# Kernel optimization log

Hardware: AMD Instinct MI355X
Metric: run time of the kernel (lower is better)

The kernel has to match this reference:

```python
import jax, jax.numpy as jnp
import numpy as np

N = 100000
E = 1600000
IN_F = 128
H_F = 128


def _sage_layer(h, weights, src, dst, W_self, b_self, W_neigh):
    # message: w_e * h[src]  -> [E, F]
    m = h[src] * weights[:, None]
    # segment-mean over destination nodes (DGL fn.mean divides by in-degree)
    s = jax.ops.segment_sum(m, dst, num_segments=N)
    deg = jax.ops.segment_sum(jnp.ones((E,), h.dtype), dst, num_segments=N)
    neigh = s / jnp.maximum(deg, 1.0)[:, None]
    # DGL SAGEConv('mean'): fc_self(h) + fc_neigh(neigh); bias lives in fc_self
    return h @ W_self.T + b_self + neigh @ W_neigh.T


def setup_inputs() -> dict:
    key = jax.random.key(0)
    ks = jax.random.split(key, 10)
    scale_in = 1.0 / np.sqrt(IN_F)
    scale_h = 1.0 / np.sqrt(H_F)
    return {
        "in_feat": jax.random.normal(ks[0], (N, IN_F), jnp.float32),
        "weights": jax.random.uniform(ks[1], (E,), jnp.float32),
        "src": jax.random.randint(ks[2], (E,), 0, N),
        "dst": jax.random.randint(ks[3], (E,), 0, N),
        "W_self1": jax.random.normal(ks[4], (H_F, IN_F), jnp.float32) * scale_in,
        "b_self1": jnp.zeros((H_F,), jnp.float32),
        "W_neigh1": jax.random.normal(ks[5], (H_F, IN_F), jnp.float32) * scale_in,
        "W_self2": jax.random.normal(ks[6], (H_F, H_F), jnp.float32) * scale_h,
        "b_self2": jnp.zeros((H_F,), jnp.float32),
        "W_neigh2": jax.random.normal(ks[7], (H_F, H_F), jnp.float32) * scale_h,
    }


def reference(in_feat, weights, src, dst, W_self1, b_self1, W_neigh1, W_self2, b_self2, W_neigh2):
    h = _sage_layer(in_feat, weights, src, dst, W_self1, b_self1, W_neigh1)
    h = jax.nn.relu(h)
    h = _sage_layer(h, weights, src, dst, W_self2, b_self2, W_neigh2)
    return h
```

## Files before the change

### kernel.cpp

```cpp
#include <hip/hip_runtime.h>


#define NN 100000
#define NE 1600000
#define F 128

#define SCAN_BS 1024
#define NBLK ((NN + SCAN_BS - 1) / SCAN_BS)

#define NPB 512
#define NBUK ((NN + NPB - 1) / NPB)
#define EPB 4096
#define NBLK3 ((NE + EPB - 1) / EPB)

static const size_t CNT_OFF   = 0;
static const size_t ROW_OFF   = 400000;
static const size_t BSUM_OFF  = 800016;
static const size_t EDGE_OFF  = 804112;
static const size_t WCAT1_OFF = 13604112;
static const size_t WCAT2_OFF = 13669648;
static const size_t SBF_OFF   = 13735184;
static const size_t H1BF_OFF  = 39335184;
static const size_t WS_NEED   = 64935184;

static const size_t FB_S_OFF = 524288;

typedef __attribute__((ext_vector_type(8))) short short8;
typedef __attribute__((ext_vector_type(4))) float float4v;

__device__ __forceinline__ float bf2f(unsigned int u16) {
    unsigned int x = u16 << 16;
    float f;
    __builtin_memcpy(&f, &x, 4);
    return f;
}
__device__ __forceinline__ unsigned int f2bf(float f) {
    unsigned int x;
    __builtin_memcpy(&x, &f, 4);
    unsigned int r = x + 0x7FFFu + ((x >> 16) & 1u);
    return r >> 16;
}


__global__ __launch_bounds__(256) void count_kernel(const int* __restrict__ dst,
                                                    int* __restrict__ cnt) {
    int e = blockIdx.x * 256 + threadIdx.x;
    if (e < NE) atomicAdd(&cnt[dst[e]], 1);
}

__global__ __launch_bounds__(256) void scan1_kernel(const int* __restrict__ cnt,
                                                    int* __restrict__ part,
                                                    int* __restrict__ bsum) {
    __shared__ int ts[256];
    int t = threadIdx.x;
    int base = blockIdx.x * SCAN_BS + t * 4;
    int c0 = (base     < NN) ? cnt[base]     : 0;
    int c1 = (base + 1 < NN) ? cnt[base + 1] : 0;
    int c2 = (base + 2 < NN) ? cnt[base + 2] : 0;
    int c3 = (base + 3 < NN) ? cnt[base + 3] : 0;
    int sum = c0 + c1 + c2 + c3;
    ts[t] = sum;
    __syncthreads();
    for (int off = 1; off < 256; off <<= 1) {
        int u = (t >= off) ? ts[t - off] : 0;
        __syncthreads();
        ts[t] += u;
        __syncthreads();
    }
    int excl = ts[t] - sum;
    if (t == 255) bsum[blockIdx.x] = ts[255];
    if (base     < NN) part[base]     = excl;
    if (base + 1 < NN) part[base + 1] = excl + c0;
    if (base + 2 < NN) part[base + 2] = excl + c0 + c1;
    if (base + 3 < NN) part[base + 3] = excl + c0 + c1 + c2;
}

__global__ __launch_bounds__(128) void scan2_kernel(int* __restrict__ bsum) {
    __shared__ int ts[128];
    int t = threadIdx.x;
    int v = (t < NBLK) ? bsum[t] : 0;
    ts[t] = v;
    __syncthreads();
    for (int off = 1; off < 128; off <<= 1) {
        int u = (t >= off) ? ts[t - off] : 0;
        __syncthreads();
        ts[t] += u;
        __syncthreads();
    }
    if (t < NBLK) bsum[t] = ts[t] - v;
}

__global__ __launch_bounds__(256) void scan3_kernel(int* __restrict__ part,
                                                    const int* __restrict__ bsum) {
    int i = blockIdx.x * 256 + threadIdx.x;
    if (i < NN) part[i] += bsum[i / SCAN_BS];
    if (i == 0) part[NN] = NE;
}


__global__ void bcur_init(const int* __restrict__ row, int* __restrict__ bcur) {
    int b = threadIdx.x;
    if (b < NBUK) bcur[b] = row[b * NPB];
}

__global__ __launch_bounds__(256) void bscatter(const int* __restrict__ src,
                                                const int* __restrict__ dst,
                                                const float* __restrict__ w,
                                                int* __restrict__ bcur,
                                                int2* __restrict__ ebuf) {
    __shared__ int2 rec[EPB];
    __shared__ unsigned char bid[EPB];
    __shared__ int hist[NBUK];
    __shared__ int gbase[NBUK];
    __shared__ int cur[NBUK];

    int t = threadIdx.x;
    for (int i = t; i < NBUK; i += 256) { hist[i] = 0; cur[i] = 0; }
    __syncthreads();

    int base_e = blockIdx.x * EPB;
#pragma unroll
    for (int i = 0; i < 16; i++) {
        int idx = i * 256 + t;
        int e = base_e + idx;
        if (e < NE) {
            int d = dst[e];
            int b = d >> 9;
            int2 r;
            r.x = src[e] | ((d & 511) << 17);
            r.y = __float_as_int(w[e]);
            rec[idx] = r;
            bid[idx] = (unsigned char)b;
            atomicAdd(&hist[b], 1);
        } else {
            bid[idx] = 255;
        }
    }
    __syncthreads();

    for (int i = t; i < NBUK; i += 256)
        if (hist[i] > 0) gbase[i] = atomicAdd(&bcur[i], hist[i]);
    __syncthreads();

#pragma unroll
    for (int i = 0; i < 16; i++) {
        int idx = i * 256 + t;
        int b = bid[idx];
        if (b != 255) {
            int r = atomicAdd(&cur[b], 1);
            ebuf[gbase[b] + r] = rec[idx];
        }
    }
}

__global__ __launch_bounds__(256) void fine_fill(const int* __restrict__ row,
                                                 const int2* __restrict__ ebuf,
                                                 int2* __restrict__ edge) {
    __shared__ int lcur[NPB];
    int b = blockIdx.x;
    int t = threadIdx.x;
    int n0 = b * NPB;
    int n1 = min(n0 + NPB, NN);
    for (int i = t; i < n1 - n0; i += 256) lcur[i] = row[n0 + i];
    __syncthreads();
    int beg = row[n0], end = row[n1];
    for (int e = beg + t; e < end; e += 256) {
        int2 r = ebuf[e];
        int dl = (r.x >> 17) & 511;
        int pos = atomicAdd(&lcur[dl], 1);
        int2 o;
        o.x = r.x & 0x1FFFF;
        o.y = r.y;
        edge[pos] = o;
    }
}


__global__ __launch_bounds__(256) void wprep_kernel(const float* __restrict__ Ws,
                                                    const float* __restrict__ Wn,
                                                    unsigned short* __restrict__ wcat) {
    int idx = blockIdx.x * 256 + threadIdx.x;
    if (idx >= 128 * 256) return;
    int n = idx >> 8, k = idx & 255;
    float v = (k < 128) ? Ws[n * 128 + k] : Wn[n * 128 + (k - 128)];
    wcat[idx] = (unsigned short)f2bf(v);
}

__global__ __launch_bounds__(256) void conv_bf16(const float* __restrict__ in,
                                                 unsigned short* __restrict__ outbf) {
    size_t base = ((size_t)blockIdx.x * 256 + threadIdx.x) * 8;
    float4 a = *(const float4*)(in + base);
    float4 b = *(const float4*)(in + base + 4);
    uint4 p;
    p.x = f2bf(a.x) | (f2bf(a.y) << 16);
    p.y = f2bf(a.z) | (f2bf(a.w) << 16);
    p.z = f2bf(b.x) | (f2bf(b.y) << 16);
    p.w = f2bf(b.z) | (f2bf(b.w) << 16);
    *(uint4*)(outbf + base) = p;
}

__global__ __launch_bounds__(256) void gather_packed(const unsigned short* __restrict__ h,
                                                     const int* __restrict__ row,
                                                     const int2* __restrict__ edge,
                                                     unsigned short* __restrict__ sbf) {
    int t = threadIdx.x;
    int lane = t & 63;
    int n = blockIdx.x * 4 + (t >> 6);
    int beg = __builtin_amdgcn_readfirstlane(row[n]);
    int end = __builtin_amdgcn_readfirstlane(row[n + 1]);
    const unsigned int* hp = (const unsigned int*)h;

    float ax = 0.0f, ay = 0.0f;
    int e = beg;
    for (; e + 7 < end; e += 8) {
        int2 m[8];
#pragma unroll
        for (int i = 0; i < 8; i++) m[i] = edge[e + i];
        unsigned int p[8];
#pragma unroll
        for (int i = 0; i < 8; i++) p[i] = hp[(size_t)m[i].x * 64 + lane];
#pragma unroll
        for (int i = 0; i < 8; i++) {
            float wf = __int_as_float(m[i].y);
            ax += wf * bf2f(p[i] & 0xFFFFu);
            ay += wf * bf2f(p[i] >> 16);
        }
    }
    for (; e < end; e++) {
        int2 m0 = edge[e];
        unsigned int p0 = hp[(size_t)m0.x * 64 + lane];
        float wf = __int_as_float(m0.y);
        ax += wf * bf2f(p0 & 0xFFFFu);
        ay += wf * bf2f(p0 >> 16);
    }
    float invd = 1.0f / fmaxf((float)(end - beg), 1.0f);
    unsigned int outp = f2bf(ax * invd) | (f2bf(ay * invd) << 16);
    ((unsigned int*)sbf)[(size_t)n * 64 + lane] = outp;
}


__global__ __launch_bounds__(256) void mfma_gemm(
    const unsigned short* self_bf,
    const unsigned short* __restrict__ sbf,
    const unsigned short* __restrict__ wcat,
    const float* __restrict__ bias,
    unsigned short* out_bf,
    float* __restrict__ out_f32)
{
    __shared__ unsigned short Bs[128][256];

    int t = threadIdx.x;
    int l = t & 63;
    int w = t >> 6;
    int base = blockIdx.x * 128;
    int lane16 = l & 15;
    int quad = l >> 4;

    int r0 = base + w * 32 + lane16;
    int r1 = r0 + 16;
    int r0c = min(r0, NN - 1);
    int r1c = min(r1, NN - 1);

    const unsigned short* s0p = self_bf + (size_t)r0c * F + quad * 8;
    const unsigned short* s1p = self_bf + (size_t)r1c * F + quad * 8;
    const unsigned short* n0p = sbf     + (size_t)r0c * F + quad * 8;
    const unsigned short* n1p = sbf     + (size_t)r1c * F + quad * 8;

    short8 A0[8], A1[8];
#pragma unroll
    for (int kk = 0; kk < 4; kk++) {
        A0[kk]     = *(const short8*)(s0p + kk * 32);
        A1[kk]     = *(const short8*)(s1p + kk * 32);
        A0[4 + kk] = *(const short8*)(n0p + kk * 32);
        A1[4 + kk] = *(const short8*)(n1p + kk * 32);
    }

    uint4 sv[16];
#pragma unroll
    for (int i = 0; i < 16; i++) {
        int idx = i * 256 + t;
        sv[i] = *(const uint4*)(wcat + idx * 8);
    }
#pragma unroll
    for (int i = 0; i < 16; i++) {
        int idx = i * 256 + t;
        int r = idx >> 5;
        int c = (idx & 31) * 8;
        *(uint4*)&Bs[r][c] = sv[i];
    }
    __syncthreads();

    float4v acc0[8], acc1[8];
#pragma unroll
    for (int ct = 0; ct < 8; ct++) {
        acc0[ct] = (float4v){0.f, 0.f, 0.f, 0.f};
        acc1[ct] = (float4v){0.f, 0.f, 0.f, 0.f};
    }

#pragma unroll
    for (int half = 0; half < 2; half++) {
#pragma unroll
        for (int kk = 0; kk < 4; kk++) {
#pragma unroll
            for (int ct = 0; ct < 8; ct++) {
                short8 b = *(const short8*)&Bs[ct * 16 + lane16][half * 128 + kk * 32 + quad * 8];
                acc0[ct] = __builtin_amdgcn_mfma_f32_16x16x32_bf16(A0[half * 4 + kk], b, acc0[ct], 0, 0, 0);
                acc1[ct] = __builtin_amdgcn_mfma_f32_16x16x32_bf16(A1[half * 4 + kk], b, acc1[ct], 0, 0, 0);
            }
        }
    }

    int rowb0 = base + w * 32 + quad * 4;
    int rowb1 = rowb0 + 16;
#pragma unroll
    for (int ct = 0; ct < 8; ct++) {
        int col = ct * 16 + lane16;
        float bc = bias[col];
#pragma unroll
        for (int r = 0; r < 4; r++) {
            int g0 = rowb0 + r, g1 = rowb1 + r;
            float v0 = acc0[ct][r] + bc;
            float v1 = acc1[ct][r] + bc;
            if (out_bf) {
                v0 = fmaxf(v0, 0.0f);
                v1 = fmaxf(v1, 0.0f);
                if (g0 < NN) out_bf[(size_t)g0 * F + col] = (unsigned short)f2bf(v0);
                if (g1 < NN) out_bf[(size_t)g1 * F + col] = (unsigned short)f2bf(v1);
            } else {
                if (g0 < NN) out_f32[(size_t)g0 * F + col] = v0;
                if (g1 < NN) out_f32[(size_t)g1 * F + col] = v1;
            }
        }
    }
}


__global__ __launch_bounds__(256) void scatter_kernel(const float* __restrict__ h,
                                                      const float* __restrict__ w,
                                                      const int* __restrict__ src,
                                                      const int* __restrict__ dst,
                                                      float* __restrict__ s,
                                                      float* __restrict__ deg,
                                                      int add_deg) {
    int e = blockIdx.x * 4 + (threadIdx.x >> 6);
    int lane = threadIdx.x & 63;
    int sn = src[e];
    int dn = dst[e];
    float wf = w[e];
    float2 p = *(const float2*)(h + (size_t)sn * F + lane * 2);
    float* sp = s + (size_t)dn * F + lane * 2;
    unsafeAtomicAdd(sp,     wf * p.x);
    unsafeAtomicAdd(sp + 1, wf * p.y);
    if (add_deg && lane == 0) unsafeAtomicAdd(&deg[dn], 1.0f);
}

__global__ __launch_bounds__(256) void sage_gemm(const float* h,
                                                 const float* __restrict__ s,
                                                 const float* deg,
                                                 const float* __restrict__ Ws,
                                                 const float* __restrict__ bias,
                                                 const float* __restrict__ Wn,
                                                 float* out,
                                                 int relu) {
    __shared__ float xs[16][F];
    __shared__ float invd[16];
    int t = threadIdx.x;
    int j = t & 127;
    int g = t >> 7;
    int base = blockIdx.x * 16;
    for (int idx = t; idx < 16 * 32; idx += 256) {
        int n = idx >> 5, kq = idx & 31;
        *(float4*)&xs[n][kq * 4] = *(const float4*)(h + (size_t)(base + n) * F + kq * 4);
    }
    if (t < 16) invd[t] = deg ? 1.0f / fmaxf(deg[base + t], 1.0f) : 1.0f;
    __syncthreads();
    float acc[8];
#pragma unroll
    for (int i = 0; i < 8; i++) acc[i] = 0.0f;
    for (int kc = 0; kc < F; kc += 4) {
        float4 wv = *(const float4*)(Ws + j * F + kc);
#pragma unroll
        for (int i = 0; i < 8; i++) {
            const float* xr = &xs[g * 8 + i][kc];
            acc[i] += xr[0] * wv.x + xr[1] * wv.y + xr[2] * wv.z + xr[3] * wv.w;
        }
    }
    __syncthreads();
    for (int idx = t; idx < 16 * 32; idx += 256) {
        int n = idx >> 5, kq = idx & 31;
        float4 sv = *(const float4*)(s + (size_t)(base + n) * F + kq * 4);
        float iv = invd[n];
        xs[n][kq * 4]     = sv.x * iv;
        xs[n][kq * 4 + 1] = sv.y * iv;
        xs[n][kq * 4 + 2] = sv.z * iv;
        xs[n][kq * 4 + 3] = sv.w * iv;
    }
    __syncthreads();
    for (int kc = 0; kc < F; kc += 4) {
        float4 wv = *(const float4*)(Wn + j * F + kc);
#pragma unroll
        for (int i = 0; i < 8; i++) {
            const float* xr = &xs[g * 8 + i][kc];
            acc[i] += xr[0] * wv.x + xr[1] * wv.y + xr[2] * wv.z + xr[3] * wv.w;
        }
    }
    float bj = bias[j];
#pragma unroll
    for (int i = 0; i < 8; i++) {
        int n = base + g * 8 + i;
        float v = acc[i] + bj;
        if (relu) v = fmaxf(v, 0.0f);
        out[(size_t)n * F + j] = v;
    }
}

extern "C" void kernel_launch(void* const* d_in, const int* in_sizes, int n_in,
                              void* d_out, int out_size, void* d_ws, size_t ws_size,
                              hipStream_t stream) {
    const float* in_feat = (const float*)d_in[0];
    const float* weights = (const float*)d_in[1];
    const int* src = (const int*)d_in[2];
    const int* dst = (const int*)d_in[3];
    const float* Ws1 = (const float*)d_in[4];
    const float* b1  = (const float*)d_in[5];
    const float* Wn1 = (const float*)d_in[6];
    const float* Ws2 = (const float*)d_in[7];
    const float* b2  = (const float*)d_in[8];
    const float* Wn2 = (const float*)d_in[9];
    float* out = (float*)d_out;

    if (ws_size >= WS_NEED) {
        int* cnt    = (int*)((char*)d_ws + CNT_OFF);
        int* row    = (int*)((char*)d_ws + ROW_OFF);
        int* bsum   = (int*)((char*)d_ws + BSUM_OFF);
        int2* edge  = (int2*)((char*)d_ws + EDGE_OFF);
        unsigned short* wcat1 = (unsigned short*)((char*)d_ws + WCAT1_OFF);
        unsigned short* wcat2 = (unsigned short*)((char*)d_ws + WCAT2_OFF);
        unsigned short* sbf   = (unsigned short*)((char*)d_ws + SBF_OFF);
        int2* ebuf  = (int2*)((char*)d_ws + SBF_OFF);
        unsigned short* hbf   = (unsigned short*)((char*)d_ws + H1BF_OFF);

        hipMemsetAsync(cnt, 0, 400000, stream);
        count_kernel<<<(NE + 255) / 256, 256, 0, stream>>>(dst, cnt);
        scan1_kernel<<<NBLK, 256, 0, stream>>>(cnt, row, bsum);
        scan2_kernel<<<1, 128, 0, stream>>>(bsum);
        scan3_kernel<<<(NN + 255) / 256, 256, 0, stream>>>(row, bsum);
        bcur_init<<<1, 256, 0, stream>>>(row, cnt);
        bscatter<<<NBLK3, 256, 0, stream>>>(src, dst, weights, cnt, ebuf);
        fine_fill<<<NBUK, 256, 0, stream>>>(row, ebuf, edge);
        wprep_kernel<<<128, 256, 0, stream>>>(Ws1, Wn1, wcat1);
        wprep_kernel<<<128, 256, 0, stream>>>(Ws2, Wn2, wcat2);
        conv_bf16<<<6250, 256, 0, stream>>>(in_feat, hbf);

        gather_packed<<<NN / 4, 256, 0, stream>>>(hbf, row, edge, sbf);
        mfma_gemm<<<(NN + 127) / 128, 256, 0, stream>>>(hbf, sbf, wcat1, b1, hbf, nullptr);
        gather_packed<<<NN / 4, 256, 0, stream>>>(hbf, row, edge, sbf);
        mfma_gemm<<<(NN + 127) / 128, 256, 0, stream>>>(hbf, sbf, wcat2, b2, nullptr, out);
    } else {
        float* deg = (float*)d_ws;
        float* s   = (float*)((char*)d_ws + FB_S_OFF);
        hipMemsetAsync(d_ws, 0, FB_S_OFF + (size_t)NN * F * 4, stream);
        scatter_kernel<<<NE / 4, 256, 0, stream>>>(in_feat, weights, src, dst, s, deg, 1);
        sage_gemm<<<NN / 16, 256, 0, stream>>>(in_feat, s, deg, Ws1, b1, Wn1, out, 1);
        hipMemsetAsync(s, 0, (size_t)NN * F * 4, stream);
        scatter_kernel<<<NE / 4, 256, 0, stream>>>(out, weights, src, dst, s, deg, 0);
        sage_gemm<<<NN / 16, 256, 0, stream>>>(out, s, deg, Ws2, b2, Wn2, out, 0);
    }
}
```

Baseline: 457.2 us.

## Fuse prep launches, shrink sort buckets, and use direct-to-LDS swizzled weight loads in GEMM

Several changes at once. The bucket sort now uses 128-node buckets instead of 512, and bucket cursors are written inside scan3, which removes the bcur_init launch. The two weight-prep launches are merged into one. The GEMM now runs 512 threads per block over 256 rows, loads weights straight into LDS with global_load_lds using an XOR swizzle to avoid bank conflicts, and loads A fragments per half to cut register pressure. Smaller buckets mean more launched blocks and more global atomics in bscatter, and the changed GEMM shape alters occupancy.

```diff
diff --git a/kernel.cpp b/kernel.cpp
--- a/kernel.cpp
+++ b/kernel.cpp
@@ -8,7 +8,8 @@
 #define SCAN_BS 1024
 #define NBLK ((NN + SCAN_BS - 1) / SCAN_BS)
 
-#define NPB 512
+#define NPB 128
+#define NPB_BITS 7
 #define NBUK ((NN + NPB - 1) / NPB)
 #define EPB 4096
 #define NBLK3 ((NE + EPB - 1) / EPB)
@@ -41,6 +42,12 @@
     return r >> 16;
 }
 
+__device__ __forceinline__ void gload_lds16(const unsigned short* g, unsigned short* l) {
+    __builtin_amdgcn_global_load_lds(
+        (const __attribute__((address_space(1))) unsigned int*)(g),
+        (__attribute__((address_space(3))) unsigned int*)(l), 16, 0, 0);
+}
+
 
 __global__ __launch_bounds__(256) void count_kernel(const int* __restrict__ dst,
                                                     int* __restrict__ cnt) {
@@ -91,17 +98,17 @@
 }
 
 __global__ __launch_bounds__(256) void scan3_kernel(int* __restrict__ part,
-                                                    const int* __restrict__ bsum) {
+                                                    const int* __restrict__ bsum,
+                                                    int* __restrict__ bcur) {
     int i = blockIdx.x * 256 + threadIdx.x;
-    if (i < NN) part[i] += bsum[i / SCAN_BS];
+    if (i < NN) {
+        int v = part[i] + bsum[i / SCAN_BS];
+        part[i] = v;
+        if ((i & (NPB - 1)) == 0) bcur[i >> NPB_BITS] = v;
+    }
     if (i == 0) part[NN] = NE;
 }
 
-
-__global__ void bcur_init(const int* __restrict__ row, int* __restrict__ bcur) {
-    int b = threadIdx.x;
-    if (b < NBUK) bcur[b] = row[b * NPB];
-}
 
 __global__ __launch_bounds__(256) void bscatter(const int* __restrict__ src,
                                                 const int* __restrict__ dst,
@@ -109,7 +116,7 @@
                                                 int* __restrict__ bcur,
                                                 int2* __restrict__ ebuf) {
     __shared__ int2 rec[EPB];
-    __shared__ unsigned char bid[EPB];
+    __shared__ unsigned short bid[EPB];
     __shared__ int hist[NBUK];
     __shared__ int gbase[NBUK];
     __shared__ int cur[NBUK];
@@ -125,15 +132,15 @@
         int e = base_e + idx;
         if (e < NE) {
             int d = dst[e];
-            int b = d >> 9;
+            int b = d >> NPB_BITS;
             int2 r;
-            r.x = src[e] | ((d & 511) << 17);
+            r.x = src[e] | ((d & (NPB - 1)) << 17);
             r.y = __float_as_int(w[e]);
             rec[idx] = r;
-            bid[idx] = (unsigned char)b;
+            bid[idx] = (unsigned short)b;
             atomicAdd(&hist[b], 1);
         } else {
-            bid[idx] = 255;
+            bid[idx] = 0xFFFFu;
         }
     }
     __syncthreads();
@@ -146,7 +153,7 @@
     for (int i = 0; i < 16; i++) {
         int idx = i * 256 + t;
         int b = bid[idx];
-        if (b != 255) {
+        if (b != 0xFFFFu) {
             int r = atomicAdd(&cur[b], 1);
             ebuf[gbase[b] + r] = rec[idx];
         }
@@ -166,7 +173,7 @@
     int beg = row[n0], end = row[n1];
     for (int e = beg + t; e < end; e += 256) {
         int2 r = ebuf[e];
-        int dl = (r.x >> 17) & 511;
+        int dl = (r.x >> 17) & (NPB - 1);
         int pos = atomicAdd(&lcur[dl], 1);
         int2 o;
         o.x = r.x & 0x1FFFF;
@@ -176,14 +183,21 @@
 }
 
 
-__global__ __launch_bounds__(256) void wprep_kernel(const float* __restrict__ Ws,
-                                                    const float* __restrict__ Wn,
-                                                    unsigned short* __restrict__ wcat) {
+__global__ __launch_bounds__(256) void wprep_kernel(const float* __restrict__ Ws1,
+                                                    const float* __restrict__ Wn1,
+                                                    const float* __restrict__ Ws2,
+                                                    const float* __restrict__ Wn2,
+                                                    unsigned short* __restrict__ wcat1,
+                                                    unsigned short* __restrict__ wcat2) {
     int idx = blockIdx.x * 256 + threadIdx.x;
-    if (idx >= 128 * 256) return;
-    int n = idx >> 8, k = idx & 255;
+    int which = idx >> 15;
+    int j = idx & 32767;
+    int n = j >> 8, k = j & 255;
+    const float* Ws = which ? Ws2 : Ws1;
+    const float* Wn = which ? Wn2 : Wn1;
     float v = (k < 128) ? Ws[n * 128 + k] : Wn[n * 128 + (k - 128)];
-    wcat[idx] = (unsigned short)f2bf(v);
+    unsigned short* o = which ? wcat2 : wcat1;
+    o[j] = (unsigned short)f2bf(v);
 }
 
 __global__ __launch_bounds__(256) void conv_bf16(const float* __restrict__ in,
@@ -239,7 +253,7 @@
 }
 
 
-__global__ __launch_bounds__(256) void mfma_gemm(
+__global__ __launch_bounds__(512, 4) void mfma_gemm(
     const unsigned short* self_bf,
     const unsigned short* __restrict__ sbf,
     const unsigned short* __restrict__ wcat,
@@ -252,44 +266,26 @@
     int t = threadIdx.x;
     int l = t & 63;
     int w = t >> 6;
-    int base = blockIdx.x * 128;
+    int base = blockIdx.x * 256;
     int lane16 = l & 15;
     int quad = l >> 4;
+    int swz = (lane16 & 7) << 3;
+
+    unsigned short* lbase = &Bs[0][0];
+#pragma unroll
+    for (int i = 0; i < 8; i++) {
+        int idx = i * 512 + t;
+        int r = idx >> 5;
+        int cb = (idx & 31) << 4;
+        int sb = cb ^ ((r & 7) << 4);
+        gload_lds16(wcat + r * 256 + (sb >> 1), lbase + idx * 8);
+    }
 
     int r0 = base + w * 32 + lane16;
     int r1 = r0 + 16;
     int r0c = min(r0, NN - 1);
     int r1c = min(r1, NN - 1);
 
-    const unsigned short* s0p = self_bf + (size_t)r0c * F + quad * 8;
-    const unsigned short* s1p = self_bf + (size_t)r1c * F + quad * 8;
-    const unsigned short* n0p = sbf     + (size_t)r0c * F + quad * 8;
-    const unsigned short* n1p = sbf     + (size_t)r1c * F + quad * 8;
-
-    short8 A0[8], A1[8];
-#pragma unroll
-    for (int kk = 0; kk < 4; kk++) {
-        A0[kk]     = *(const short8*)(s0p + kk * 32);
-        A1[kk]     = *(const short8*)(s1p + kk * 32);
-        A0[4 + kk] = *(const short8*)(n0p + kk * 32);
-        A1[4 + kk] = *(const short8*)(n1p + kk * 32);
-    }
-
-    uint4 sv[16];
-#pragma unroll
-    for (int i = 0; i < 16; i++) {
-        int idx = i * 256 + t;
-        sv[i] = *(const uint4*)(wcat + idx * 8);
-    }
-#pragma unroll
-    for (int i = 0; i < 16; i++) {
-        int idx = i * 256 + t;
-        int r = idx >> 5;
-        int c = (idx & 31) * 8;
-        *(uint4*)&Bs[r][c] = sv[i];
-    }
-    __syncthreads();
-
     float4v acc0[8], acc1[8];
 #pragma unroll
     for (int ct = 0; ct < 8; ct++) {
@@ -297,15 +293,28 @@
         acc1[ct] = (float4v){0.f, 0.f, 0.f, 0.f};
     }
 
+    __syncthreads();
+
 #pragma unroll
     for (int half = 0; half < 2; half++) {
+        const unsigned short* srcb = (half == 0) ? self_bf : sbf;
+        const unsigned short* p0 = srcb + (size_t)r0c * F + quad * 8;
+        const unsigned short* p1 = srcb + (size_t)r1c * F + quad * 8;
+        short8 Ah0[4], Ah1[4];
 #pragma unroll
         for (int kk = 0; kk < 4; kk++) {
+            Ah0[kk] = *(const short8*)(p0 + kk * 32);
+            Ah1[kk] = *(const short8*)(p1 + kk * 32);
+        }
+#pragma unroll
+        for (int kk = 0; kk < 4; kk++) {
 #pragma unroll
             for (int ct = 0; ct < 8; ct++) {
-                short8 b = *(const short8*)&Bs[ct * 16 + lane16][half * 128 + kk * 32 + quad * 8];
-                acc0[ct] = __builtin_amdgcn_mfma_f32_16x16x32_bf16(A0[half * 4 + kk], b, acc0[ct], 0, 0, 0);
-                acc1[ct] = __builtin_amdgcn_mfma_f32_16x16x32_bf16(A1[half * 4 + kk], b, acc1[ct], 0, 0, 0);
+                int r = ct * 16 + lane16;
+                int col = half * 128 + kk * 32 + quad * 8;
+                short8 b = *(const short8*)(lbase + (size_t)r * 256 + (col ^ swz));
+                acc0[ct] = __builtin_amdgcn_mfma_f32_16x16x32_bf16(Ah0[kk], b, acc0[ct], 0, 0, 0);
+                acc1[ct] = __builtin_amdgcn_mfma_f32_16x16x32_bf16(Ah1[kk], b, acc1[ct], 0, 0, 0);
             }
         }
     }
@@ -444,18 +453,16 @@
         count_kernel<<<(NE + 255) / 256, 256, 0, stream>>>(dst, cnt);
         scan1_kernel<<<NBLK, 256, 0, stream>>>(cnt, row, bsum);
         scan2_kernel<<<1, 128, 0, stream>>>(bsum);
-        scan3_kernel<<<(NN + 255) / 256, 256, 0, stream>>>(row, bsum);
-        bcur_init<<<1, 256, 0, stream>>>(row, cnt);
+        scan3_kernel<<<(NN + 255) / 256, 256, 0, stream>>>(row, bsum, cnt);
         bscatter<<<NBLK3, 256, 0, stream>>>(src, dst, weights, cnt, ebuf);
         fine_fill<<<NBUK, 256, 0, stream>>>(row, ebuf, edge);
-        wprep_kernel<<<128, 256, 0, stream>>>(Ws1, Wn1, wcat1);
-        wprep_kernel<<<128, 256, 0, stream>>>(Ws2, Wn2, wcat2);
+        wprep_kernel<<<256, 256, 0, stream>>>(Ws1, Wn1, Ws2, Wn2, wcat1, wcat2);
         conv_bf16<<<6250, 256, 0, stream>>>(in_feat, hbf);
 
         gather_packed<<<NN / 4, 256, 0, stream>>>(hbf, row, edge, sbf);
-        mfma_gemm<<<(NN + 127) / 128, 256, 0, stream>>>(hbf, sbf, wcat1, b1, hbf, nullptr);
+        mfma_gemm<<<(NN + 255) / 256, 512, 0, stream>>>(hbf, sbf, wcat1, b1, hbf, nullptr);
         gather_packed<<<NN / 4, 256, 0, stream>>>(hbf, row, edge, sbf);
-        mfma_gemm<<<(NN + 127) / 128, 256, 0, stream>>>(hbf, sbf, wcat2, b2, nullptr, out);
+        mfma_gemm<<<(NN + 255) / 256, 512, 0, stream>>>(hbf, sbf, wcat2, b2, nullptr, out);
     } else {
         float* deg = (float*)d_ws;
         float* s   = (float*)((char*)d_ws + FB_S_OFF);
```

Result: faster. 428.4 us, median of 2 (-6.3%).
